# Kernel optimization log

Measured on AMD Instinct MI355X. Metric: run time of the kernel, lower is better.

The kernel has to match this reference:

```python
import jax, jax.numpy as jnp
import numpy as np

T, D, L, H = 512, 256, 256, 512  # tokens, embed dim, lstm dims, hidden units


def _lstm(x, W, U, b):
    """Keras-style LSTM over x [T, Din] -> hidden states [T, L].
    Gate order i, f, g(cell), o; sigmoid recurrent activations, tanh cell."""
    Ldim = U.shape[0]

    def step(carry, xt):
        h, c = carry
        z = xt @ W + h @ U + b  # [4L]
        i, f, g, o = jnp.split(z, 4)
        i = jax.nn.sigmoid(i)
        f = jax.nn.sigmoid(f)
        g = jnp.tanh(g)
        o = jax.nn.sigmoid(o)
        c = f * c + i * g
        h = o * jnp.tanh(c)
        return (h, c), h

    h0 = jnp.zeros((Ldim,), x.dtype)
    _, hs = jax.lax.scan(step, (h0, h0), x)
    return hs


def setup_inputs() -> dict:
    key = jax.random.key(0)
    ks = jax.random.split(key, 16)

    def p(k, shape):
        # Glorot-like small init
        fan = shape[0] + shape[-1]
        return jax.random.normal(k, shape, jnp.float32) * np.float32(np.sqrt(2.0 / fan))

    return {
        "embeddings": jax.random.normal(ks[0], (1, T, D), jnp.float32),
        "W_f1": p(ks[1], (D, 4 * L)), "U_f1": p(ks[2], (L, 4 * L)), "b_f1": jnp.zeros((4 * L,), jnp.float32),
        "W_b1": p(ks[3], (D, 4 * L)), "U_b1": p(ks[4], (L, 4 * L)), "b_b1": jnp.zeros((4 * L,), jnp.float32),
        "W_f2": p(ks[5], (2 * L, 4 * L)), "U_f2": p(ks[6], (L, 4 * L)), "b_f2": jnp.zeros((4 * L,), jnp.float32),
        "W_b2": p(ks[7], (2 * L, 4 * L)), "U_b2": p(ks[8], (L, 4 * L)), "b_b2": jnp.zeros((4 * L,), jnp.float32),
        "FOH": p(ks[9], (2 * L, H)),
        "FOM": p(ks[10], (2 * L, H)),
        "hidBias": p(ks[11], (1, H)),
        "outLayer": p(ks[12], (H, 1)),
        "outBias": p(ks[13], (1, 1)),
    }


def reference(embeddings, W_f1, U_f1, b_f1, W_b1, U_b1, b_b1,
              W_f2, U_f2, b_f2, W_b2, U_b2, b_b2,
              FOH, FOM, hidBias, outLayer, outBias):
    x = embeddings[0]  # [T, D]
    # --- FirstBiLSTMModule ---
    rf1 = _lstm(x, W_f1, U_f1, b_f1)            # forward LSTM over sequence
    rb1 = _lstm(x[::-1], W_b1, U_b1, b_b1)      # backward LSTM over reversed sequence
    # concatenate_layers: pair forward step i with backward step T-1-i
    v = jnp.concatenate([rf1, rb1[::-1]], axis=-1)  # [T, 2L]
    # --- NextBiLSTMModule ---
    rf2 = _lstm(v, W_f2, U_f2, b_f2)
    rb2 = _lstm(v[::-1], W_b2, U_b2, b_b2)
    hcat = jnp.concatenate([rf2, rb2[::-1]], axis=-1)  # [T, 2L] per-token concat
    # --- ConcatHeadModule.__evaluate (hidden2_units == 0 path) ---
    headfov = hcat @ FOH  # [T, H]
    modfov = hcat @ FOM   # [T, H]
    # pairwise: activation(headfov_i + modfov_j + hidBias) @ outLayer + outBias
    act = jnp.tanh(headfov[:, None, :] + modfov[None, :, :] + hidBias[0])  # [T, T, H]
    scores = jnp.einsum('ijh,ho->ij', act, outLayer) + outBias[0, 0]       # [T, T]
    return scores
```

## Files before the change

### kernel.cpp

```cpp
#include <hip/hip_runtime.h>
#include <hip/hip_bf16.h>


typedef _Float16 h2v __attribute__((ext_vector_type(2)));

#define BC(x) __builtin_bit_cast(h2v, (x))

__device__ __forceinline__ float fdot2f(h2v a, h2v b, float c) {
#if __has_builtin(__builtin_amdgcn_fdot2)
    return __builtin_amdgcn_fdot2(a, b, c, false);
#else
    return c + (float)a[0] * (float)b[0] + (float)a[1] * (float)b[1];
#endif
}

__global__ __launch_bounds__(256) void prep4(const float* __restrict__ U0,
                                             const float* __restrict__ U1,
                                             const float* __restrict__ U2,
                                             const float* __restrict__ U3,
                                             unsigned int* __restrict__ Uf) {
    int which = blockIdx.x >> 9;
    const float* U = which == 0 ? U0 : which == 1 ? U1 : which == 2 ? U2 : U3;
    unsigned int* out = Uf + which * 131072;
    int idx = (blockIdx.x & 511) * 256 + threadIdx.x;
    int k2 = idx >> 10, col = idx & 1023;
    union { _Float16 h[2]; unsigned int u; } p;
    p.h[0] = (_Float16)U[(2 * k2) * 1024 + col];
    p.h[1] = (_Float16)U[(2 * k2 + 1) * 1024 + col];
    out[idx] = p.u;
}

__global__ __launch_bounds__(256) void gemm_cat(
        const float* __restrict__ A0, const float* __restrict__ A1, int halfK,
        const float* __restrict__ Bz0, const float* __restrict__ Bz1,
        const float* __restrict__ bias0, const float* __restrict__ bias1,
        float* __restrict__ C0, float* __restrict__ C1,
        int M, int N, int K, int revZ1) {
    const float* B = blockIdx.z ? Bz1 : Bz0;
    const float* bias = blockIdx.z ? bias1 : bias0;
    float* C = blockIdx.z ? C1 : C0;
    int rev = blockIdx.z ? revZ1 : 0;

    __shared__ float sA[16][65];
    __shared__ float sB[16][65];
    int tid = threadIdx.x;
    int bm = blockIdx.y * 64, bn = blockIdx.x * 64;
    int tx = tid & 15, ty = tid >> 4;
    float acc[4][4] = {};
    for (int k0 = 0; k0 < K; k0 += 16) {
#pragma unroll
        for (int l = 0; l < 4; l++) {
            int flat = tid + 256 * l;
            int ml = flat >> 4, kk = flat & 15;
            int row = bm + ml;
            int rr = rev ? M - 1 - row : row;
            int kcol = k0 + kk;
            float val = (kcol < halfK) ? A0[rr * halfK + kcol]
                                       : A1[(M - 1 - rr) * halfK + kcol - halfK];
            sA[kk][ml] = val;
        }
#pragma unroll
        for (int l = 0; l < 4; l++) {
            int flat = tid + 256 * l;
            int kk = flat >> 6, nl = flat & 63;
            sB[kk][nl] = B[(k0 + kk) * N + bn + nl];
        }
        __syncthreads();
#pragma unroll
        for (int kk = 0; kk < 16; kk++) {
            float a[4], b[4];
#pragma unroll
            for (int i = 0; i < 4; i++) a[i] = sA[kk][ty + 16 * i];
#pragma unroll
            for (int j = 0; j < 4; j++) b[j] = sB[kk][tx + 16 * j];
#pragma unroll
            for (int i = 0; i < 4; i++)
#pragma unroll
                for (int j = 0; j < 4; j++) acc[i][j] += a[i] * b[j];
        }
        __syncthreads();
    }
#pragma unroll
    for (int i = 0; i < 4; i++) {
        int r = bm + ty + 16 * i;
#pragma unroll
        for (int j = 0; j < 4; j++) {
            int cidx = bn + tx + 16 * j;
            float bv = bias ? bias[cidx] : 0.f;
            C[r * N + cidx] = acc[i][j] + bv;
        }
    }
}

#define KLDS 36
#define KREG 92

#define CHUNKS(X) X(0) X(1) X(2) X(3) X(4) X(5) X(6) X(7) X(8) X(9) X(10) \
    X(11) X(12) X(13) X(14) X(15) X(16) X(17) X(18) X(19) X(20) X(21) X(22)

__global__ __attribute__((amdgpu_flat_work_group_size(1024, 1024)))
void lstm_two(
        const unsigned int* __restrict__ Ua, const unsigned int* __restrict__ Ub,
        const float* __restrict__ Pa, const float* __restrict__ Pb,
        float* __restrict__ Oa, float* __restrict__ Ob) {
    const unsigned int* U = blockIdx.x ? Ub : Ua;
    const float* P = blockIdx.x ? Pb : Pa;
    float* O = blockIdx.x ? Ob : Oa;

    __shared__ unsigned int sU[KLDS * 1024];
    __shared__ __align__(16) _Float16 sH[256];
    __shared__ float sZ[1024];

    int t = threadIdx.x;

    for (int i = t; i < KLDS * 1024; i += 1024) sU[i] = U[i];

#define DECLQ(i) uint4 uq##i;
    CHUNKS(DECLQ)
#undef DECLQ
#define LOADQ(i) uq##i = make_uint4(U[(KLDS + 4 * i + 0) * 1024 + t], \
                                    U[(KLDS + 4 * i + 1) * 1024 + t], \
                                    U[(KLDS + 4 * i + 2) * 1024 + t], \
                                    U[(KLDS + 4 * i + 3) * 1024 + t]);
    CHUNKS(LOADQ)
#undef LOADQ

    float c = 0.f;
    if (t < 256) sH[t] = (_Float16)0.f;
    __syncthreads();

    const uint4* hp4 = (const uint4*)sH;
    float pc = P[t];
    for (int step = 0; step < 512; step++) {
        float pn = pc;
        if (step < 511) pn = P[(step + 1) * 1024 + t];
        float acc0 = pc, acc1 = 0.f;

#pragma unroll
        for (int ch = 0; ch < 9; ch++) {
            uint4 hc = hp4[ch];
            acc0 = fdot2f(BC(hc.x), BC(sU[(4 * ch + 0) * 1024 + t]), acc0);
            acc1 = fdot2f(BC(hc.y), BC(sU[(4 * ch + 1) * 1024 + t]), acc1);
            acc0 = fdot2f(BC(hc.z), BC(sU[(4 * ch + 2) * 1024 + t]), acc0);
            acc1 = fdot2f(BC(hc.w), BC(sU[(4 * ch + 3) * 1024 + t]), acc1);
        }
#define DOTQ(i) { uint4 hc = hp4[9 + i];                     \
        acc0 = fdot2f(BC(hc.x), BC(uq##i.x), acc0);          \
        acc1 = fdot2f(BC(hc.y), BC(uq##i.y), acc1);          \
        acc0 = fdot2f(BC(hc.z), BC(uq##i.z), acc0);          \
        acc1 = fdot2f(BC(hc.w), BC(uq##i.w), acc1); }
        CHUNKS(DOTQ)
#undef DOTQ

        float z = acc0 + acc1;
        float a;
        if ((t >> 8) == 2) a = 1.f - 2.f / (1.f + __expf(2.f * z));
        else               a = 1.f / (1.f + __expf(-z));
        sZ[t] = a;
        __syncthreads();
        if (t < 256) {
            float ig = sZ[t], fg = sZ[256 + t], gg = sZ[512 + t], og = sZ[768 + t];
            c = fg * c + ig * gg;
            float h = og * (1.f - 2.f / (1.f + __expf(2.f * c)));
            O[step * 256 + t] = h;
            sH[t] = (_Float16)h;
        }
        __syncthreads();
        pc = pn;
    }
}

__global__ __launch_bounds__(256) void head_kernel(const float* __restrict__ HF,
                                                   const float* __restrict__ MF,
                                                   const float* __restrict__ w,
                                                   const float* __restrict__ outb,
                                                   float* __restrict__ S) {
    int i = blockIdx.x;
    __shared__ float sHF[512], sW[512];
    int tid = threadIdx.x;
    sHF[tid] = HF[i * 512 + tid];
    sHF[tid + 256] = HF[i * 512 + 256 + tid];
    sW[tid] = w[tid];
    sW[tid + 256] = w[tid + 256];
    __syncthreads();
    int lane = tid & 63, wv = tid >> 6;
    float ob = outb[0];
    for (int j = wv; j < 512; j += 4) {
        const float* mf = MF + j * 512;
        float acc = 0.f;
#pragma unroll
        for (int r = 0; r < 8; r++) {
            int h = lane + 64 * r;
            float x = sHF[h] + mf[h];
            acc += sW[h] * (1.f - 2.f / (1.f + __expf(2.f * x)));
        }
#pragma unroll
        for (int off = 32; off; off >>= 1) acc += __shfl_down(acc, off);
        if (lane == 0) S[i * 512 + j] = acc + ob;
    }
}

extern "C" void kernel_launch(void* const* d_in, const int* in_sizes, int n_in,
                              void* d_out, int out_size, void* d_ws, size_t ws_size,
                              hipStream_t stream) {
    const float* emb      = (const float*)d_in[0];
    const float* W_f1     = (const float*)d_in[1];
    const float* U_f1     = (const float*)d_in[2];
    const float* b_f1     = (const float*)d_in[3];
    const float* W_b1     = (const float*)d_in[4];
    const float* U_b1     = (const float*)d_in[5];
    const float* b_b1     = (const float*)d_in[6];
    const float* W_f2     = (const float*)d_in[7];
    const float* U_f2     = (const float*)d_in[8];
    const float* b_f2     = (const float*)d_in[9];
    const float* W_b2     = (const float*)d_in[10];
    const float* U_b2     = (const float*)d_in[11];
    const float* b_b2     = (const float*)d_in[12];
    const float* FOH      = (const float*)d_in[13];
    const float* FOM      = (const float*)d_in[14];
    const float* hidBias  = (const float*)d_in[15];
    const float* outLayer = (const float*)d_in[16];
    const float* outBias  = (const float*)d_in[17];
    float* out = (float*)d_out;

    unsigned int* uf = (unsigned int*)d_ws;
    unsigned int* uf_f1 = uf;
    unsigned int* uf_b1 = uf + 131072;
    unsigned int* uf_f2 = uf + 262144;
    unsigned int* uf_b2 = uf + 393216;
    float* f = (float*)d_ws + 524288;
    float* P1f = f;
    float* P1b = f + 524288;
    float* P2f = f + 1048576;
    float* P2b = f + 1572864;
    float* rf1 = f + 2097152;
    float* rb1 = f + 2228224;
    float* rf2 = f + 2359296;
    float* rb2 = f + 2490368;
    float* HFb  = f + 2621440;
    float* MFb  = f + 2883584;

    prep4<<<2048, 256, 0, stream>>>(U_f1, U_b1, U_f2, U_b2, uf);

    gemm_cat<<<dim3(16, 8, 2), 256, 0, stream>>>(
        emb, emb, 256, W_f1, W_b1, b_f1, b_b1, P1f, P1b, 512, 1024, 256, 1);

    lstm_two<<<2, 1024, 0, stream>>>(uf_f1, uf_b1, P1f, P1b, rf1, rb1);

    gemm_cat<<<dim3(16, 8, 2), 256, 0, stream>>>(
        rf1, rb1, 256, W_f2, W_b2, b_f2, b_b2, P2f, P2b, 512, 1024, 512, 1);

    lstm_two<<<2, 1024, 0, stream>>>(uf_f2, uf_b2, P2f, P2b, rf2, rb2);

    gemm_cat<<<dim3(8, 8, 2), 256, 0, stream>>>(
        rf2, rb2, 256, FOH, FOM, hidBias, nullptr, HFb, MFb, 512, 512, 512, 0);

    head_kernel<<<512, 256, 0, stream>>>(HFb, MFb, outLayer, outBias, out);
}
```

Baseline: 2.818 ms.

## Split each LSTM direction across four workgroups with global atomic step sync

Replaces the single 1024-thread workgroup per direction with four 512-thread workgroups per direction. Each workgroup owns 64 hidden units and keeps its recurrent-weight slice entirely in registers, with two half-K partial dot products per gate column. Hidden states are exchanged each step through a global buffer, guarded by per-step atomic counters and a spin wait, and the counters are cleared by a memset before each launch. This spreads the per-step matvec across more CUs and removes the LDS-resident weight reads, at the cost of a cross-CU synchronization and global round trip on every one of the 512 steps.

```diff
diff --git a/kernel.cpp b/kernel.cpp
--- a/kernel.cpp
+++ b/kernel.cpp
@@ -92,78 +92,90 @@
     }
 }
 
-#define KLDS 36
-#define KREG 92
-
-#define CHUNKS(X) X(0) X(1) X(2) X(3) X(4) X(5) X(6) X(7) X(8) X(9) X(10) \
-    X(11) X(12) X(13) X(14) X(15) X(16) X(17) X(18) X(19) X(20) X(21) X(22)
-
-__global__ __attribute__((amdgpu_flat_work_group_size(1024, 1024)))
-void lstm_two(
-        const unsigned int* __restrict__ Ua, const unsigned int* __restrict__ Ub,
-        const float* __restrict__ Pa, const float* __restrict__ Pb,
-        float* __restrict__ Oa, float* __restrict__ Ob) {
-    const unsigned int* U = blockIdx.x ? Ub : Ua;
-    const float* P = blockIdx.x ? Pb : Pa;
-    float* O = blockIdx.x ? Ob : Oa;
-
-    __shared__ unsigned int sU[KLDS * 1024];
-    __shared__ __align__(16) _Float16 sH[256];
-    __shared__ float sZ[1024];
+__global__ __launch_bounds__(512, 2) void lstm_sync(
+        const unsigned int* __restrict__ Uf,
+        const float* __restrict__ P,
+        float* __restrict__ Out,
+        float* __restrict__ Hb,
+        int* __restrict__ cnt) {
+    int dir = blockIdx.x >> 2;
+    int g   = blockIdx.x & 3;
+    const unsigned int* U = Uf + dir * 131072;
+    const float* Pd = P + dir * (512 * 1024);
+    float* Od = Out + dir * (512 * 256);
+    int* cn = cnt + dir * 512;
 
     int t = threadIdx.x;
-
-    for (int i = t; i < KLDS * 1024; i += 1024) sU[i] = U[i];
-
-#define DECLQ(i) uint4 uq##i;
-    CHUNKS(DECLQ)
-#undef DECLQ
-#define LOADQ(i) uq##i = make_uint4(U[(KLDS + 4 * i + 0) * 1024 + t], \
-                                    U[(KLDS + 4 * i + 1) * 1024 + t], \
-                                    U[(KLDS + 4 * i + 2) * 1024 + t], \
-                                    U[(KLDS + 4 * i + 3) * 1024 + t]);
-    CHUNKS(LOADQ)
-#undef LOADQ
-
-    float c = 0.f;
-    if (t < 256) sH[t] = (_Float16)0.f;
+    int lc = t & 255;
+    int hh = t >> 8;
+    int G = lc >> 6, u = lc & 63;
+    int gc = G * 256 + g * 64 + u;
+
+    __shared__ unsigned sHp[128];
+    __shared__ float sPart[512];
+    __shared__ float sG[256];
+
+    uint4 uq[16];
+#pragma unroll
+    for (int i = 0; i < 16; i++) {
+        int kp = hh * 64 + 4 * i;
+        uq[i].x = U[(kp + 0) * 1024 + gc];
+        uq[i].y = U[(kp + 1) * 1024 + gc];
+        uq[i].z = U[(kp + 2) * 1024 + gc];
+        uq[i].w = U[(kp + 3) * 1024 + gc];
+    }
+
+    if (t < 128) sHp[t] = 0u;
+    float cst = 0.f;
     __syncthreads();
 
-    const uint4* hp4 = (const uint4*)sH;
-    float pc = P[t];
-    for (int step = 0; step < 512; step++) {
-        float pn = pc;
-        if (step < 511) pn = P[(step + 1) * 1024 + t];
-        float acc0 = pc, acc1 = 0.f;
-
-#pragma unroll
-        for (int ch = 0; ch < 9; ch++) {
-            uint4 hc = hp4[ch];
-            acc0 = fdot2f(BC(hc.x), BC(sU[(4 * ch + 0) * 1024 + t]), acc0);
-            acc1 = fdot2f(BC(hc.y), BC(sU[(4 * ch + 1) * 1024 + t]), acc1);
-            acc0 = fdot2f(BC(hc.z), BC(sU[(4 * ch + 2) * 1024 + t]), acc0);
-            acc1 = fdot2f(BC(hc.w), BC(sU[(4 * ch + 3) * 1024 + t]), acc1);
-        }
-#define DOTQ(i) { uint4 hc = hp4[9 + i];                     \
-        acc0 = fdot2f(BC(hc.x), BC(uq##i.x), acc0);          \
-        acc1 = fdot2f(BC(hc.y), BC(uq##i.y), acc1);          \
-        acc0 = fdot2f(BC(hc.z), BC(uq##i.z), acc0);          \
-        acc1 = fdot2f(BC(hc.w), BC(uq##i.w), acc1); }
-        CHUNKS(DOTQ)
-#undef DOTQ
-
-        float z = acc0 + acc1;
-        float a;
-        if ((t >> 8) == 2) a = 1.f - 2.f / (1.f + __expf(2.f * z));
-        else               a = 1.f / (1.f + __expf(-z));
-        sZ[t] = a;
+    float pc = (t < 256) ? Pd[gc] : 0.f;
+    for (int s = 0; s < 512; s++) {
+        float pn = (s < 511 && t < 256) ? Pd[(s + 1) * 1024 + gc] : 0.f;
+
+        float a0 = 0.f, a1 = 0.f;
+#pragma unroll
+        for (int i = 0; i < 16; i++) {
+            uint4 hc = ((const uint4*)sHp)[hh * 16 + i];
+            a0 = fdot2f(BC(hc.x), BC(uq[i].x), a0);
+            a1 = fdot2f(BC(hc.y), BC(uq[i].y), a1);
+            a0 = fdot2f(BC(hc.z), BC(uq[i].z), a0);
+            a1 = fdot2f(BC(hc.w), BC(uq[i].w), a1);
+        }
+        sPart[t] = a0 + a1;
         __syncthreads();
         if (t < 256) {
-            float ig = sZ[t], fg = sZ[256 + t], gg = sZ[512 + t], og = sZ[768 + t];
-            c = fg * c + ig * gg;
-            float h = og * (1.f - 2.f / (1.f + __expf(2.f * c)));
-            O[step * 256 + t] = h;
-            sH[t] = (_Float16)h;
+            float z = pc + sPart[t] + sPart[t + 256];
+            sG[t] = (G == 2) ? 1.f - 2.f / (1.f + __expf(2.f * z))
+                             : 1.f / (1.f + __expf(-z));
+        }
+        __syncthreads();
+        int par = s & 1;
+        if (t < 64) {
+            float ig = sG[t], fg = sG[64 + t], gg = sG[128 + t], og = sG[192 + t];
+            cst = fg * cst + ig * gg;
+            float h = og * (1.f - 2.f / (1.f + __expf(2.f * cst)));
+            Od[s * 256 + g * 64 + t] = h;
+            Hb[(par * 2 + dir) * 256 + g * 64 + t] = h;
+        }
+        if (t == 0) {
+            __threadfence();
+            __hip_atomic_fetch_add(&cn[s], 1, __ATOMIC_RELEASE,
+                                   __HIP_MEMORY_SCOPE_AGENT);
+            while (__hip_atomic_load(&cn[s], __ATOMIC_ACQUIRE,
+                                     __HIP_MEMORY_SCOPE_AGENT) < 4)
+                __builtin_amdgcn_s_sleep(1);
+        }
+        __syncthreads();
+        if (t < 128) {
+            unsigned long long w = __hip_atomic_load(
+                (const unsigned long long*)&Hb[(par * 2 + dir) * 256 + 2 * t],
+                __ATOMIC_RELAXED, __HIP_MEMORY_SCOPE_AGENT);
+            float2 hf = __builtin_bit_cast(float2, w);
+            union { _Float16 h[2]; unsigned u_; } pk;
+            pk.h[0] = (_Float16)hf.x;
+            pk.h[1] = (_Float16)hf.y;
+            sHp[t] = pk.u_;
         }
         __syncthreads();
         pc = pn;
@@ -224,36 +236,35 @@
     float* out = (float*)d_out;
 
     unsigned int* uf = (unsigned int*)d_ws;
-    unsigned int* uf_f1 = uf;
-    unsigned int* uf_b1 = uf + 131072;
-    unsigned int* uf_f2 = uf + 262144;
-    unsigned int* uf_b2 = uf + 393216;
     float* f = (float*)d_ws + 524288;
-    float* P1f = f;
-    float* P1b = f + 524288;
-    float* P2f = f + 1048576;
-    float* P2b = f + 1572864;
-    float* rf1 = f + 2097152;
-    float* rb1 = f + 2228224;
-    float* rf2 = f + 2359296;
-    float* rb2 = f + 2490368;
+    float* P1   = f;
+    float* P2   = f + 1048576;
+    float* R1   = f + 2097152;
+    float* R2   = f + 2359296;
     float* HFb  = f + 2621440;
     float* MFb  = f + 2883584;
+    float* Hb   = f + 3145728;
+    int*   cnt  = (int*)(f + 3146752);
 
     prep4<<<2048, 256, 0, stream>>>(U_f1, U_b1, U_f2, U_b2, uf);
 
     gemm_cat<<<dim3(16, 8, 2), 256, 0, stream>>>(
-        emb, emb, 256, W_f1, W_b1, b_f1, b_b1, P1f, P1b, 512, 1024, 256, 1);
-
-    lstm_two<<<2, 1024, 0, stream>>>(uf_f1, uf_b1, P1f, P1b, rf1, rb1);
+        emb, emb, 256, W_f1, W_b1, b_f1, b_b1, P1, P1 + 524288,
+        512, 1024, 256, 1);
+
+    hipMemsetAsync(cnt, 0, 2 * 512 * sizeof(int), stream);
+    lstm_sync<<<8, 512, 0, stream>>>(uf, P1, R1, Hb, cnt);
 
     gemm_cat<<<dim3(16, 8, 2), 256, 0, stream>>>(
-        rf1, rb1, 256, W_f2, W_b2, b_f2, b_b2, P2f, P2b, 512, 1024, 512, 1);
-
-    lstm_two<<<2, 1024, 0, stream>>>(uf_f2, uf_b2, P2f, P2b, rf2, rb2);
+        R1, R1 + 131072, 256, W_f2, W_b2, b_f2, b_b2, P2, P2 + 524288,
+        512, 1024, 512, 1);
+
+    hipMemsetAsync(cnt, 0, 2 * 512 * sizeof(int), stream);
+    lstm_sync<<<8, 512, 0, stream>>>(uf + 262144, P2, R2, Hb, cnt);
 
     gemm_cat<<<dim3(8, 8, 2), 256, 0, stream>>>(
-        rf2, rb2, 256, FOH, FOM, hidBias, nullptr, HFb, MFb, 512, 512, 512, 0);
+        R2, R2 + 131072, 256, FOH, FOM, hidBias, nullptr, HFb, MFb,
+        512, 512, 512, 0);
 
     head_kernel<<<512, 256, 0, stream>>>(HFb, MFb, outLayer, outBias, out);
 }
```

Result: no change. 2.778 ms (-1.4%).
